# Performance work log

Hardware: AMD Instinct MI355X
Metric: run time of the kernel (lower is better)

The kernel has to match this reference:

```python
import jax, jax.numpy as jnp
import numpy as np

# dims
B, N, D = 256, 77, 768     # batch, CLIP tokens, token dim
K, Dn, H = 16, 768, 8      # nodes, node dim, heads
HID, L = 512, 2            # edge-MLP hidden, num GNN layers


def setup_inputs() -> dict:
    key = jax.random.key(0)
    ks = jax.random.split(key, 12)
    g = lambda k, shape, s=0.02: (jax.random.normal(k, shape, jnp.float32) * s)
    return {
        "w": jax.random.normal(ks[0], (B, N, D), jnp.float32),
        "token_mask": jax.random.randint(ks[1], (B, N), 0, 2).astype(jnp.int32),
        "node_queries": g(ks[2], (1, K, Dn)),
        "Wq": g(ks[3], (Dn, Dn)), "bq": jnp.zeros((Dn,), jnp.float32),
        "Wk": g(ks[4], (D, Dn)),  "bk": jnp.zeros((Dn,), jnp.float32),
        "Wv": g(ks[5], (D, Dn)),  "bv": jnp.zeros((Dn,), jnp.float32),
        "We1": g(ks[6], (2 * Dn, HID)), "be1": jnp.zeros((HID,), jnp.float32),
        "We2": g(ks[7], (HID, 1)),      "be2": jnp.zeros((1,), jnp.float32),
        "fuse_gate": jnp.float32(0.0),
        "Wg": g(ks[8], (L, Dn, Dn)), "bg": jnp.zeros((L, Dn), jnp.float32),
    }


def _edge_logits(V, We1, be1, We2, be2):
    # edge_mlp(cat[Vi, Vj]) without materializing [B,K,K,2Dn]:
    # split first linear into the Vi-half and Vj-half of its weight.
    hi = V @ We1[:Dn]   # [B,K,HID]
    hj = V @ We1[Dn:]   # [B,K,HID]
    h = jax.nn.relu(hi[:, :, None, :] + hj[:, None, :, :] + be1)  # [B,K,K,HID]
    return jnp.einsum('bijh,h->bij', h, We2[:, 0]) + be2[0]       # [B,K,K]


def _forward(w, node_queries, Wq, bq, Wk, bk, Wv, bv,
             We1, be1, We2, be2, fuse_gate, Wg, bg, token_mask):
    q = jnp.broadcast_to(node_queries, (B, K, Dn))
    Q = q @ Wq + bq        # [B,K,Dn]
    Kt = w @ Wk + bk       # [B,N,Dn]
    Vt = w @ Wv + bv       # [B,N,Dn]
    # per-head dot products summed over heads == full Dn dot product
    scale = (Dn // H) ** -0.5
    scores = jnp.einsum('bkd,bnd->bkn', Q, Kt) * scale  # [B,K,N]
    pad = (token_mask == 0)[:, None, :]                 # [B,1,N]
    scores = jnp.where(pad, jnp.finfo(scores.dtype).min, scores)
    # softmax over K per token (transpose to [B,N,K])
    S = jax.nn.softmax(jnp.swapaxes(scores, 1, 2), axis=-1)  # [B,N,K]
    V = jnp.einsum('bnk,bnd->bkd', S, Vt)                    # [B,K,Dn]
    gate = jax.nn.sigmoid(fuse_gate)
    V = (1.0 - gate) * V + gate * q
    # pre-GNN edge logits, then relational GNN refinement
    E = _edge_logits(V, We1, be1, We2, be2)
    A = jax.nn.softmax(E, axis=-1)  # [B,K,K], fixed across layers
    for l in range(L):
        msg = jnp.einsum('bij,bjd->bid', A, V @ Wg[l] + bg[l])
        V = V + jax.nn.relu(msg)
    # post-GNN edge logits
    E = _edge_logits(V, We1, be1, We2, be2)
    return S, V, E


def reference(w, token_mask, node_queries, Wq, bq, Wk, bk, Wv, bv,
              We1, be1, We2, be2, fuse_gate, Wg, bg):
    return _forward(w, node_queries, Wq, bq, Wk, bk, Wv, bv,
                    We1, be1, We2, be2, fuse_gate, Wg, bg, token_mask)
```

## Files before the change

### kernel.cpp

```cpp
#include <hip/hip_runtime.h>

typedef unsigned short u16;
typedef __attribute__((ext_vector_type(8))) short short8;
typedef __attribute__((ext_vector_type(4))) float f32x4;

#define DEV static __device__ __forceinline__

DEV float bf2f(u16 u) { return __uint_as_float(((unsigned)u) << 16); }
DEV u16 f2bf(float f) {
  unsigned u = __float_as_uint(f);
  return (u16)((u + 0x7fffu + ((u >> 16) & 1u)) >> 16);
}

DEV void cp16(void* lds, const void* g) {
  __builtin_amdgcn_global_load_lds(
      (const __attribute__((address_space(1))) unsigned int*)g,
      (__attribute__((address_space(3))) unsigned int*)lds, 16, 0, 0);
}

DEV int xcd_swz() {
  int bid = blockIdx.x;
  int cpx = gridDim.x >> 3;
  return (bid & 7) * cpx + (bid >> 3);
}


__global__ __launch_bounds__(256) void tcast_all(const float* __restrict__ Wv,
                                                 const float* __restrict__ We1,
                                                 const float* __restrict__ Wg,
                                                 u16* __restrict__ WvT,
                                                 u16* __restrict__ We1T,
                                                 u16* __restrict__ WgT) {
  __shared__ float tile[32][33];
  const float* src; u16* dst; int C;
  switch (blockIdx.z) {
    case 0: src = Wv;           dst = WvT;           C = 768; break;
    case 1: src = We1;          dst = We1T;          C = 512; break;
    case 2: src = We1 + 393216; dst = We1T + 393216; C = 512; break;
    case 3: src = Wg;           dst = WgT;           C = 768; break;
    default: src = Wg + 589824; dst = WgT + 589824;  C = 768; break;
  }
  int r0 = blockIdx.y * 32, c0 = blockIdx.x * 32;
  if (c0 >= C) return;
  int tr = threadIdx.x >> 5, tc = threadIdx.x & 31;
#pragma unroll
  for (int rr = 0; rr < 4; ++rr)
    tile[tr + rr * 8][tc] = src[(size_t)(r0 + tr + rr * 8) * C + c0 + tc];
  __syncthreads();
#pragma unroll
  for (int rr = 0; rr < 4; ++rr)
    dst[(size_t)(c0 + tr + rr * 8) * 768 + r0 + tc] = f2bf(tile[tc][tr + rr * 8]);
}

__global__ __launch_bounds__(256) void q_part(const float* __restrict__ nq,
                                              const float* __restrict__ Wq,
                                              float* __restrict__ Qpart) {
  int gid = blockIdx.x * 256 + threadIdx.x;
  int s = blockIdx.y;
  int k = gid / 768, d = gid % 768;
  const float* nr = nq + k * 768 + s * 96;
  const float* wp = Wq + (size_t)(s * 96) * 768 + d;
  float s0 = 0.f, s1 = 0.f, s2 = 0.f, s3 = 0.f;
#pragma unroll
  for (int c = 0; c < 96; c += 4) {
    s0 += nr[c + 0] * wp[(size_t)(c + 0) * 768];
    s1 += nr[c + 1] * wp[(size_t)(c + 1) * 768];
    s2 += nr[c + 2] * wp[(size_t)(c + 2) * 768];
    s3 += nr[c + 3] * wp[(size_t)(c + 3) * 768];
  }
  Qpart[(size_t)s * 12288 + gid] = (s0 + s1) + (s2 + s3);
}

__global__ __launch_bounds__(256) void q_reduce(const float* __restrict__ Qpart,
                                                const float* __restrict__ bq,
                                                float* __restrict__ Qf) {
  int gid = blockIdx.x * 256 + threadIdx.x;
  int d = gid % 768;
  float s = bq[d];
#pragma unroll
  for (int i = 0; i < 8; ++i) s += Qpart[(size_t)i * 12288 + gid];
  Qf[gid] = s;
}

__global__ __launch_bounds__(256) void pt_kernel(const float* __restrict__ Qf,
                                                 const float* __restrict__ Wk,
                                                 const float* __restrict__ bk,
                                                 u16* __restrict__ PT16,
                                                 float* __restrict__ qb) {
  int t = threadIdx.x;
  if (blockIdx.x == 48) {
    int k = t >> 4, j = t & 15;
    const float* q = Qf + k * 768 + j * 48;
    const float* bp = bk + j * 48;
    float s = 0.f;
#pragma unroll
    for (int d = 0; d < 48; d += 4) {
      f32x4 qv = *(const f32x4*)&q[d];
      f32x4 bv4 = *(const f32x4*)&bp[d];
      s += qv[0] * bv4[0] + qv[1] * bv4[1] + qv[2] * bv4[2] + qv[3] * bv4[3];
    }
#pragma unroll
    for (int off = 1; off < 16; off <<= 1) s += __shfl_xor(s, off);
    if (j == 0) qb[k] = s;
    return;
  }
  int gid = blockIdx.x * 256 + t;
  int c = gid >> 4, k = gid & 15;
  const float* wr = Wk + (size_t)c * 768;
  const float* q = Qf + k * 768;
  float s = 0.f;
  for (int d = 0; d < 768; d += 4) {
    f32x4 wv = *(const f32x4*)&wr[d];
    f32x4 qv = *(const f32x4*)&q[d];
    s += wv[0] * qv[0] + wv[1] * qv[1] + wv[2] * qv[2] + wv[3] * qv[3];
  }
  PT16[k * 768 + c] = f2bf(s);
}

__global__ __launch_bounds__(256) void score2(const float* __restrict__ w,
                                              const u16* __restrict__ PT16,
                                              const float* __restrict__ qb,
                                              const int* __restrict__ mask,
                                              float* __restrict__ Sout) {
  __shared__ u16 Ps[16 * 776];
  int t = threadIdx.x, wave = t >> 6, lane = t & 63, l16 = lane & 15, quad = lane >> 4;
  int m0 = blockIdx.x * 64;
#pragma unroll
  for (int r = 0; r < 6; ++r) {
    int idx = t + 256 * r;
    int row = idx / 96, c8 = idx % 96;
    *(short8*)&Ps[row * 776 + c8 * 8] = *(const short8*)&PT16[row * 768 + c8 * 8];
  }
  __syncthreads();
  int row = m0 + wave * 16 + l16;
  const float* ap = w + (size_t)row * 768 + quad * 8;
  f32x4 acc = {0.f, 0.f, 0.f, 0.f};
#pragma unroll
  for (int it = 0; it < 24; ++it) {
    f32x4 a0 = *(const f32x4*)(ap + it * 32);
    f32x4 a1 = *(const f32x4*)(ap + it * 32 + 4);
    short8 fa;
#pragma unroll
    for (int e = 0; e < 4; ++e) { fa[e] = (short)f2bf(a0[e]); fa[e + 4] = (short)f2bf(a1[e]); }
    short8 fb = *(const short8*)&Ps[l16 * 776 + it * 32 + quad * 8];
    acc = __builtin_amdgcn_mfma_f32_16x16x32_bf16(fa, fb, acc, 0, 0, 0);
  }
  float qv = qb[l16];
  const float scale = 0.1020620726159658f;
#pragma unroll
  for (int r = 0; r < 4; ++r) {
    int orow = m0 + wave * 16 + quad * 4 + r;
    float s = (acc[r] + qv) * scale;
    if (mask[orow] == 0) s = -3.402823466e38f;
    float mx = s;
#pragma unroll
    for (int off = 1; off < 16; off <<= 1) mx = fmaxf(mx, __shfl_xor(mx, off));
    float e = __expf(s - mx);
    float sm = e;
#pragma unroll
    for (int off = 1; off < 16; off <<= 1) sm += __shfl_xor(sm, off);
    Sout[(size_t)orow * 16 + l16] = e / sm;
  }
}

__global__ __launch_bounds__(256) void u_kernel(const float* __restrict__ Sg,
                                                const float* __restrict__ w,
                                                u16* __restrict__ U16,
                                                float* __restrict__ sk) {
  __shared__ float Ss[1232];
  int b = blockIdx.x, t = threadIdx.x;
  int d = blockIdx.y * 256 + t;
#pragma unroll
  for (int r = 0; r < 5; ++r) {
    int idx = t + 256 * r;
    if (idx < 1232) Ss[idx] = Sg[(size_t)b * 1232 + idx];
  }
  __syncthreads();
  float a[16];
#pragma unroll
  for (int k = 0; k < 16; ++k) a[k] = 0.f;
  const float* wp = w + (size_t)b * 59136;
  for (int n = 0; n < 77; ++n) {
    float g = wp[(size_t)n * 768 + d];
    const float* sr = &Ss[n * 16];
#pragma unroll
    for (int k = 0; k < 16; ++k) a[k] += sr[k] * g;
  }
#pragma unroll
  for (int k = 0; k < 16; ++k)
    U16[(size_t)b * 12288 + (size_t)k * 768 + d] = f2bf(a[k]);
  if (blockIdx.y == 0 && t < 16) {
    float s = 0.f;
    for (int n = 0; n < 77; ++n) s += Ss[n * 16 + t];
    sk[b * 16 + t] = s;
  }
}

__global__ __launch_bounds__(256) void vgemm(const u16* __restrict__ A,
                                             const u16* __restrict__ BT,
                                             const float* __restrict__ skp,
                                             const float* __restrict__ bv,
                                             const float* __restrict__ nq,
                                             const float* __restrict__ gatep,
                                             float* __restrict__ V32,
                                             u16* __restrict__ V16) {
  __shared__ u16 As[2 * 64 * 32];
  __shared__ u16 Bs[2 * 128 * 32];
  int swz = xcd_swz();
  int mi = swz / 6, ni = swz % 6;
  int m0 = mi * 64, n0 = ni * 128;
  int t = threadIdx.x;
  int wave = t >> 6, lane = t & 63, l16 = lane & 15, quad = lane >> 4;
  int ra = wave * 16 + (lane >> 2);
  int rb1 = wave * 32 + (lane >> 2);
  int rb2 = rb1 + 16;
  int cslot = lane & 3;
  int cga = (cslot ^ ((ra >> 1) & 3)) * 8;
  int cgb1 = (cslot ^ ((rb1 >> 1) & 3)) * 8;
  int cgb2 = (cslot ^ ((rb2 >> 1) & 3)) * 8;

  const u16* Ap = A + (size_t)(m0 + ra) * 768 + cga;
  const u16* Bp1 = BT + (size_t)(n0 + rb1) * 768 + cgb1;
  const u16* Bp2 = BT + (size_t)(n0 + rb2) * 768 + cgb2;
  u16* AsW = &As[(wave * 16) * 32];
  u16* BsW1 = &Bs[(wave * 32) * 32];
  u16* BsW2 = &Bs[(wave * 32 + 16) * 32];

  f32x4 zero4 = {0.f, 0.f, 0.f, 0.f};
  f32x4 acc[4][2];
#pragma unroll
  for (int i = 0; i < 4; ++i) { acc[i][0] = zero4; acc[i][1] = zero4; }

  cp16(AsW, Ap); cp16(BsW1, Bp1); cp16(BsW2, Bp2);

  int cur = 0;
  for (int k0 = 0; k0 < 768; k0 += 32) {
    int nxt = cur ^ 1;
    if (k0 + 32 < 768) {
      cp16(AsW + nxt * 2048, Ap + k0 + 32);
      cp16(BsW1 + nxt * 4096, Bp1 + k0 + 32);
      cp16(BsW2 + nxt * 4096, Bp2 + k0 + 32);
      asm volatile("s_waitcnt vmcnt(3)" ::: "memory");
    } else {
      asm volatile("s_waitcnt vmcnt(0)" ::: "memory");
    }
    asm volatile("s_barrier" ::: "memory");
    const u16* Ab = &As[cur * 2048];
    const u16* Bb = &Bs[cur * 4096];
    short8 fa[4], fb[2];
#pragma unroll
    for (int i = 0; i < 4; ++i) {
      int R = i * 16 + l16;
      fa[i] = *(const short8*)&Ab[R * 32 + (quad ^ ((R >> 1) & 3)) * 8];
    }
#pragma unroll
    for (int j = 0; j < 2; ++j) {
      int R = wave * 32 + j * 16 + l16;
      fb[j] = *(const short8*)&Bb[R * 32 + (quad ^ ((R >> 1) & 3)) * 8];
    }
#pragma unroll
    for (int i = 0; i < 4; ++i)
#pragma unroll
      for (int j = 0; j < 2; ++j)
        acc[i][j] = __builtin_amdgcn_mfma_f32_16x16x32_bf16(fa[i], fb[j], acc[i][j], 0, 0, 0);
    asm volatile("s_barrier" ::: "memory");
    cur = nxt;
  }

  float gv = gatep[0];
  float g = 1.f / (1.f + __expf(-gv)), og = 1.f - g;
  int narr[2]; float bvj[2];
#pragma unroll
  for (int j = 0; j < 2; ++j) {
    narr[j] = n0 + wave * 32 + j * 16 + l16;
    bvj[j] = bv[narr[j]];
  }
#pragma unroll
  for (int i = 0; i < 4; ++i)
#pragma unroll
    for (int r = 0; r < 4; ++r) {
      int m = m0 + i * 16 + quad * 4 + r;
      float skv = skp[m];
      size_t mrow = (size_t)m * 768;
      const float* nqr = nq + (m & 15) * 768;
#pragma unroll
      for (int j = 0; j < 2; ++j) {
        float val = acc[i][j][r] + skv * bvj[j];
        float v = og * val + g * nqr[narr[j]];
        V32[mrow + narr[j]] = v;
        V16[mrow + narr[j]] = f2bf(v);
      }
    }
}

__global__ __launch_bounds__(256) void gemm16s(const u16* __restrict__ A,
                                               const u16* __restrict__ BT0,
                                               const float* __restrict__ bias0,
                                               u16* __restrict__ C0, int N0, int ntA,
                                               const u16* __restrict__ BT1,
                                               const float* __restrict__ bias1,
                                               u16* __restrict__ C1, int N1, int ntB,
                                               int K) {
  __shared__ u16 As[2 * 64 * 32];
  __shared__ u16 Bs[2 * 128 * 32];
  int nt = ntA + ntB;
  int swz = xcd_swz();
  int mi = swz / nt, ni = swz % nt;
  const u16* BT; const float* bias; u16* C; int N, n0;
  if (ni < ntA) { BT = BT0; bias = bias0; C = C0; N = N0; n0 = ni * 128; }
  else          { BT = BT1; bias = bias1; C = C1; N = N1; n0 = (ni - ntA) * 128; }
  int m0 = mi * 64;
  int t = threadIdx.x;
  int wave = t >> 6, lane = t & 63, l16 = lane & 15, quad = lane >> 4;
  int ra = wave * 16 + (lane >> 2);
  int rb1 = wave * 32 + (lane >> 2);
  int rb2 = rb1 + 16;
  int cslot = lane & 3;
  int cga = (cslot ^ ((ra >> 1) & 3)) * 8;
  int cgb1 = (cslot ^ ((rb1 >> 1) & 3)) * 8;
  int cgb2 = (cslot ^ ((rb2 >> 1) & 3)) * 8;

  const u16* Ap = A + (size_t)(m0 + ra) * K + cga;
  const u16* Bp1 = BT + (size_t)(n0 + rb1) * K + cgb1;
  const u16* Bp2 = BT + (size_t)(n0 + rb2) * K + cgb2;
  u16* AsW = &As[(wave * 16) * 32];
  u16* BsW1 = &Bs[(wave * 32) * 32];
  u16* BsW2 = &Bs[(wave * 32 + 16) * 32];

  f32x4 zero4 = {0.f, 0.f, 0.f, 0.f};
  f32x4 acc[4][2];
#pragma unroll
  for (int i = 0; i < 4; ++i) { acc[i][0] = zero4; acc[i][1] = zero4; }

  cp16(AsW, Ap); cp16(BsW1, Bp1); cp16(BsW2, Bp2);

  int cur = 0;
  for (int k0 = 0; k0 < K; k0 += 32) {
    int nxt = cur ^ 1;
    if (k0 + 32 < K) {
      cp16(AsW + nxt * 2048, Ap + k0 + 32);
      cp16(BsW1 + nxt * 4096, Bp1 + k0 + 32);
      cp16(BsW2 + nxt * 4096, Bp2 + k0 + 32);
      asm volatile("s_waitcnt vmcnt(3)" ::: "memory");
    } else {
      asm volatile("s_waitcnt vmcnt(0)" ::: "memory");
    }
    asm volatile("s_barrier" ::: "memory");
    const u16* Ab = &As[cur * 2048];
    const u16* Bb = &Bs[cur * 4096];
    short8 fa[4], fb[2];
#pragma unroll
    for (int i = 0; i < 4; ++i) {
      int R = i * 16 + l16;
      fa[i] = *(const short8*)&Ab[R * 32 + (quad ^ ((R >> 1) & 3)) * 8];
    }
#pragma unroll
    for (int j = 0; j < 2; ++j) {
      int R = wave * 32 + j * 16 + l16;
      fb[j] = *(const short8*)&Bb[R * 32 + (quad ^ ((R >> 1) & 3)) * 8];
    }
#pragma unroll
    for (int i = 0; i < 4; ++i)
#pragma unroll
      for (int j = 0; j < 2; ++j)
        acc[i][j] = __builtin_amdgcn_mfma_f32_16x16x32_bf16(fa[i], fb[j], acc[i][j], 0, 0, 0);
    asm volatile("s_barrier" ::: "memory");
    cur = nxt;
  }

  int narr[2]; float bvj[2];
#pragma unroll
  for (int j = 0; j < 2; ++j) {
    narr[j] = n0 + wave * 32 + j * 16 + l16;
    bvj[j] = bias ? bias[narr[j]] : 0.f;
  }
#pragma unroll
  for (int i = 0; i < 4; ++i)
#pragma unroll
    for (int r = 0; r < 4; ++r) {
      size_t mrow = (size_t)(m0 + i * 16 + quad * 4 + r) * N;
#pragma unroll
      for (int j = 0; j < 2; ++j)
        C[mrow + narr[j]] = f2bf(acc[i][j][r] + bvj[j]);
    }
}

__global__ __launch_bounds__(256) void edge_kernel(const u16* __restrict__ HIJ,
                                                   const float* __restrict__ be1,
                                                   const float* __restrict__ We2,
                                                   const float* __restrict__ be2v,
                                                   float* __restrict__ Aout,
                                                   float* __restrict__ Eout) {
  __shared__ float hiS[8 * 516];
  __shared__ float hjS[16 * 516];
  __shared__ float be1s[512];
  __shared__ float w2s[512];
  int b = blockIdx.x, ih = blockIdx.y, t = threadIdx.x;
  be1s[t] = be1[t]; be1s[t + 256] = be1[t + 256];
  w2s[t] = We2[t];  w2s[t + 256] = We2[t + 256];

#pragma unroll
  for (int r = 0; r < 6; ++r) {
    int idx = t + 256 * r;
    const u16* src;
    float* dst;
    if (idx < 512) {
      int row = idx >> 6, c8 = idx & 63;
      src = &HIJ[(size_t)(b * 16 + ih * 8 + row) * 1024 + c8 * 8];
      dst = &hiS[row * 516 + c8 * 8];
    } else {
      int k = idx - 512;
      int row = k >> 6, c8 = k & 63;
      src = &HIJ[(size_t)(b * 16 + row) * 1024 + 512 + c8 * 8];
      dst = &hjS[row * 516 + c8 * 8];
    }
    short8 hv = *(const short8*)src;
    f32x4 l0, l1;
#pragma unroll
    for (int ee = 0; ee < 4; ++ee) { l0[ee] = bf2f((u16)hv[ee]); l1[ee] = bf2f((u16)hv[ee + 4]); }
    *(f32x4*)dst = l0;
    *(f32x4*)(dst + 4) = l1;
  }
  __syncthreads();

  int i_loc = t >> 5, j = (t >> 1) & 15, hh = t & 1;
  const float* hi = &hiS[i_loc * 516 + hh * 256];
  const float* hj = &hjS[j * 516 + hh * 256];
  const float* b1 = &be1s[hh * 256];
  const float* w2 = &w2s[hh * 256];
  float e = 0.f;
#pragma unroll 2
  for (int h4 = 0; h4 < 64; ++h4) {
    f32x4 hv = *(const f32x4*)&hi[h4 * 4];
    f32x4 jv = *(const f32x4*)&hj[h4 * 4];
    f32x4 bv = *(const f32x4*)&b1[h4 * 4];
    f32x4 wv = *(const f32x4*)&w2[h4 * 4];
#pragma unroll
    for (int ee = 0; ee < 4; ++ee)
      e += fmaxf(hv[ee] + jv[ee] + bv[ee], 0.f) * wv[ee];
  }
  e += __shfl_xor(e, 1);
  e += be2v[0];

  int pair = (ih * 8 + i_loc) * 16 + j;
  if (Aout) {
    float mx = e;
#pragma unroll
    for (int off = 2; off < 32; off <<= 1) mx = fmaxf(mx, __shfl_xor(mx, off));
    float ex = __expf(e - mx);
    float sm = ex;
#pragma unroll
    for (int off = 2; off < 32; off <<= 1) sm += __shfl_xor(sm, off);
    if (hh == 0) Aout[(size_t)b * 256 + pair] = ex / sm;
  }
  if (Eout && hh == 0) Eout[(size_t)b * 256 + pair] = e;
}

__global__ __launch_bounds__(256) void combine_kernel(const float* __restrict__ Aws,
                                                      const u16* __restrict__ G,
                                                      float* __restrict__ V32,
                                                      u16* __restrict__ V16,
                                                      float* __restrict__ Vout) {
  __shared__ float Gs[16 * 260];
  __shared__ float As[256];
  int b = blockIdx.x, yc = blockIdx.y, t = threadIdx.x;
#pragma unroll
  for (int r = 0; r < 2; ++r) {
    int idx = t + 256 * r;
    int row = idx >> 5, c8 = idx & 31;
    short8 gv8 = *(const short8*)&G[(size_t)(b * 16 + row) * 768 + yc * 256 + c8 * 8];
    f32x4 l0, l1;
#pragma unroll
    for (int ee = 0; ee < 4; ++ee) { l0[ee] = bf2f((u16)gv8[ee]); l1[ee] = bf2f((u16)gv8[ee + 4]); }
    *(f32x4*)&Gs[row * 260 + c8 * 8] = l0;
    *(f32x4*)&Gs[row * 260 + c8 * 8 + 4] = l1;
  }
  As[t] = Aws[(size_t)b * 256 + t];
  __syncthreads();
  int d = yc * 256 + t;
  float gv[16];
#pragma unroll
  for (int j = 0; j < 16; ++j) gv[j] = Gs[j * 260 + t];
#pragma unroll
  for (int i = 0; i < 16; ++i) {
    float msg = 0.f;
#pragma unroll
    for (int j = 0; j < 16; ++j) msg += As[i * 16 + j] * gv[j];
    size_t idx = (size_t)b * 12288 + (size_t)i * 768 + d;
    float v = V32[idx] + fmaxf(msg, 0.f);
    V32[idx] = v;
    V16[idx] = f2bf(v);
    if (Vout) Vout[idx] = v;
  }
}

extern "C" void kernel_launch(void* const* d_in, const int* in_sizes, int n_in,
                              void* d_out, int out_size, void* d_ws, size_t ws_size,
                              hipStream_t stream) {
  const float* w    = (const float*)d_in[0];
  const int*   mask = (const int*)d_in[1];
  const float* nq   = (const float*)d_in[2];
  const float* Wq   = (const float*)d_in[3];
  const float* bq   = (const float*)d_in[4];
  const float* Wk   = (const float*)d_in[5];
  const float* bk   = (const float*)d_in[6];
  const float* Wv   = (const float*)d_in[7];
  const float* bv   = (const float*)d_in[8];
  const float* We1  = (const float*)d_in[9];
  const float* be1  = (const float*)d_in[10];
  const float* We2  = (const float*)d_in[11];
  const float* be2  = (const float*)d_in[12];
  const float* gate = (const float*)d_in[13];
  const float* Wg   = (const float*)d_in[14];
  const float* bg   = (const float*)d_in[15];

  float* ws    = (float*)d_ws;
  float* V32   = ws;
  float* Aws   = V32 + 3145728;
  float* Qpart = Aws + 65536;
  float* Qf    = Qpart + 98304;
  float* qb    = Qf + 12288;
  float* sk    = qb + 16;
  u16* PT16    = (u16*)(sk + 4096);
  u16* WvT     = PT16 + 12288;
  u16* We1T    = WvT + 589824;
  u16* WgT     = We1T + 786432;
  u16* V16     = WgT + 1179648;
  u16* U16     = V16 + 3145728;
  u16* HIJ     = U16 + 3145728;
  u16* Gws     = HIJ + 4194304;

  float* out  = (float*)d_out;
  float* Sout = out;
  float* Vout = out + 315392;
  float* Eout = out + 315392 + 3145728;

  dim3 blk(256);

  tcast_all<<<dim3(24, 24, 5), blk, 0, stream>>>(Wv, We1, Wg, WvT, We1T, WgT);
  q_part<<<dim3(48, 8), blk, 0, stream>>>(nq, Wq, Qpart);
  q_reduce<<<48, blk, 0, stream>>>(Qpart, bq, Qf);
  pt_kernel<<<49, blk, 0, stream>>>(Qf, Wk, bk, PT16, qb);

  score2<<<308, blk, 0, stream>>>(w, PT16, qb, mask, Sout);

  u_kernel<<<dim3(256, 3), blk, 0, stream>>>(Sout, w, U16, sk);
  vgemm<<<384, blk, 0, stream>>>(U16, WvT, sk, bv, nq, gate, V32, V16);

  gemm16s<<<896, blk, 0, stream>>>(V16, We1T, nullptr, HIJ, 1024, 8,
                                   WgT, bg, Gws, 768, 6, 768);
  edge_kernel<<<dim3(256, 2), blk, 0, stream>>>(HIJ, be1, We2, be2, Aws, (float*)nullptr);
  combine_kernel<<<dim3(256, 3), blk, 0, stream>>>(Aws, Gws, V32, V16, (float*)nullptr);

  gemm16s<<<384, blk, 0, stream>>>(V16, WgT + 589824, bg + 768, Gws, 768, 6,
                                   WgT + 589824, bg + 768, Gws, 768, 0, 768);
  combine_kernel<<<dim3(256, 3), blk, 0, stream>>>(Aws, Gws, V32, V16, Vout);

  gemm16s<<<512, blk, 0, stream>>>(V16, We1T, nullptr, HIJ, 1024, 8,
                                   We1T, nullptr, HIJ, 1024, 0, 768);
  edge_kernel<<<dim3(256, 2), blk, 0, stream>>>(HIJ, be1, We2, be2, (float*)nullptr, Eout);
}
```

Measured before the change: 307.9 us.

## Enlarge GEMM tiles to 128x128 with deeper prefetch pipeline

The bf16 MFMA GEMMs (V projection, edge-MLP first layer, GNN weight GEMMs) move from 64x128 tiles to 128x128 tiles, with each wave computing a 64x64 sub-block, which doubles A/B reuse per LDS load. The staging also changes: two k-steps are prefetched up front and the next stage is issued after compute, waiting with vmcnt(4). Grid sizes are halved to match. With M=4096, grids shrink to 192-448 blocks, which may underfill the 256 CUs and increases register pressure.

```diff
diff --git a/kernel.cpp b/kernel.cpp
--- a/kernel.cpp
+++ b/kernel.cpp
@@ -196,104 +196,15 @@
   }
 }
 
-__global__ __launch_bounds__(256) void vgemm(const u16* __restrict__ A,
-                                             const u16* __restrict__ BT,
-                                             const float* __restrict__ skp,
-                                             const float* __restrict__ bv,
-                                             const float* __restrict__ nq,
-                                             const float* __restrict__ gatep,
-                                             float* __restrict__ V32,
-                                             u16* __restrict__ V16) {
-  __shared__ u16 As[2 * 64 * 32];
-  __shared__ u16 Bs[2 * 128 * 32];
-  int swz = xcd_swz();
-  int mi = swz / 6, ni = swz % 6;
-  int m0 = mi * 64, n0 = ni * 128;
-  int t = threadIdx.x;
-  int wave = t >> 6, lane = t & 63, l16 = lane & 15, quad = lane >> 4;
-  int ra = wave * 16 + (lane >> 2);
-  int rb1 = wave * 32 + (lane >> 2);
-  int rb2 = rb1 + 16;
-  int cslot = lane & 3;
-  int cga = (cslot ^ ((ra >> 1) & 3)) * 8;
-  int cgb1 = (cslot ^ ((rb1 >> 1) & 3)) * 8;
-  int cgb2 = (cslot ^ ((rb2 >> 1) & 3)) * 8;
-
-  const u16* Ap = A + (size_t)(m0 + ra) * 768 + cga;
-  const u16* Bp1 = BT + (size_t)(n0 + rb1) * 768 + cgb1;
-  const u16* Bp2 = BT + (size_t)(n0 + rb2) * 768 + cgb2;
-  u16* AsW = &As[(wave * 16) * 32];
-  u16* BsW1 = &Bs[(wave * 32) * 32];
-  u16* BsW2 = &Bs[(wave * 32 + 16) * 32];
-
-  f32x4 zero4 = {0.f, 0.f, 0.f, 0.f};
-  f32x4 acc[4][2];
-#pragma unroll
-  for (int i = 0; i < 4; ++i) { acc[i][0] = zero4; acc[i][1] = zero4; }
-
-  cp16(AsW, Ap); cp16(BsW1, Bp1); cp16(BsW2, Bp2);
-
-  int cur = 0;
-  for (int k0 = 0; k0 < 768; k0 += 32) {
-    int nxt = cur ^ 1;
-    if (k0 + 32 < 768) {
-      cp16(AsW + nxt * 2048, Ap + k0 + 32);
-      cp16(BsW1 + nxt * 4096, Bp1 + k0 + 32);
-      cp16(BsW2 + nxt * 4096, Bp2 + k0 + 32);
-      asm volatile("s_waitcnt vmcnt(3)" ::: "memory");
-    } else {
-      asm volatile("s_waitcnt vmcnt(0)" ::: "memory");
-    }
-    asm volatile("s_barrier" ::: "memory");
-    const u16* Ab = &As[cur * 2048];
-    const u16* Bb = &Bs[cur * 4096];
-    short8 fa[4], fb[2];
-#pragma unroll
-    for (int i = 0; i < 4; ++i) {
-      int R = i * 16 + l16;
-      fa[i] = *(const short8*)&Ab[R * 32 + (quad ^ ((R >> 1) & 3)) * 8];
-    }
-#pragma unroll
-    for (int j = 0; j < 2; ++j) {
-      int R = wave * 32 + j * 16 + l16;
-      fb[j] = *(const short8*)&Bb[R * 32 + (quad ^ ((R >> 1) & 3)) * 8];
-    }
-#pragma unroll
-    for (int i = 0; i < 4; ++i)
-#pragma unroll
-      for (int j = 0; j < 2; ++j)
-        acc[i][j] = __builtin_amdgcn_mfma_f32_16x16x32_bf16(fa[i], fb[j], acc[i][j], 0, 0, 0);
-    asm volatile("s_barrier" ::: "memory");
-    cur = nxt;
-  }
-
-  float gv = gatep[0];
-  float g = 1.f / (1.f + __expf(-gv)), og = 1.f - g;
-  int narr[2]; float bvj[2];
-#pragma unroll
-  for (int j = 0; j < 2; ++j) {
-    narr[j] = n0 + wave * 32 + j * 16 + l16;
-    bvj[j] = bv[narr[j]];
-  }
-#pragma unroll
-  for (int i = 0; i < 4; ++i)
-#pragma unroll
-    for (int r = 0; r < 4; ++r) {
-      int m = m0 + i * 16 + quad * 4 + r;
-      float skv = skp[m];
-      size_t mrow = (size_t)m * 768;
-      const float* nqr = nq + (m & 15) * 768;
-#pragma unroll
-      for (int j = 0; j < 2; ++j) {
-        float val = acc[i][j][r] + skv * bvj[j];
-        float v = og * val + g * nqr[narr[j]];
-        V32[mrow + narr[j]] = v;
-        V16[mrow + narr[j]] = f2bf(v);
-      }
-    }
-}
-
-__global__ __launch_bounds__(256) void gemm16s(const u16* __restrict__ A,
+#define STG128(BI, KOFF)                                    \
+  do {                                                      \
+    cp16(&As[(BI) * 4096 + (wave * 32) * 32],      Ap1 + (KOFF)); \
+    cp16(&As[(BI) * 4096 + (wave * 32 + 16) * 32], Ap2 + (KOFF)); \
+    cp16(&Bs[(BI) * 4096 + (wave * 32) * 32],      Bp1 + (KOFF)); \
+    cp16(&Bs[(BI) * 4096 + (wave * 32 + 16) * 32], Bp2 + (KOFF)); \
+  } while (0)
+
+__global__ __launch_bounds__(256) void gemm128(const u16* __restrict__ A,
                                                const u16* __restrict__ BT0,
                                                const float* __restrict__ bias0,
                                                u16* __restrict__ C0, int N0, int ntA,
@@ -301,7 +212,7 @@
                                                const float* __restrict__ bias1,
                                                u16* __restrict__ C1, int N1, int ntB,
                                                int K) {
-  __shared__ u16 As[2 * 64 * 32];
+  __shared__ u16 As[2 * 128 * 32];
   __shared__ u16 Bs[2 * 128 * 32];
   int nt = ntA + ntB;
   int swz = xcd_swz();
@@ -309,79 +220,162 @@
   const u16* BT; const float* bias; u16* C; int N, n0;
   if (ni < ntA) { BT = BT0; bias = bias0; C = C0; N = N0; n0 = ni * 128; }
   else          { BT = BT1; bias = bias1; C = C1; N = N1; n0 = (ni - ntA) * 128; }
-  int m0 = mi * 64;
+  int m0 = mi * 128;
   int t = threadIdx.x;
   int wave = t >> 6, lane = t & 63, l16 = lane & 15, quad = lane >> 4;
-  int ra = wave * 16 + (lane >> 2);
-  int rb1 = wave * 32 + (lane >> 2);
-  int rb2 = rb1 + 16;
+  int wrow = (wave >> 1) * 64, wcol = (wave & 1) * 64;
+  int r1 = wave * 32 + (lane >> 2);
+  int r2 = r1 + 16;
   int cslot = lane & 3;
-  int cga = (cslot ^ ((ra >> 1) & 3)) * 8;
-  int cgb1 = (cslot ^ ((rb1 >> 1) & 3)) * 8;
-  int cgb2 = (cslot ^ ((rb2 >> 1) & 3)) * 8;
-
-  const u16* Ap = A + (size_t)(m0 + ra) * K + cga;
-  const u16* Bp1 = BT + (size_t)(n0 + rb1) * K + cgb1;
-  const u16* Bp2 = BT + (size_t)(n0 + rb2) * K + cgb2;
-  u16* AsW = &As[(wave * 16) * 32];
-  u16* BsW1 = &Bs[(wave * 32) * 32];
-  u16* BsW2 = &Bs[(wave * 32 + 16) * 32];
+  int cg1 = (cslot ^ ((r1 >> 1) & 3)) * 8;
+  int cg2 = (cslot ^ ((r2 >> 1) & 3)) * 8;
+
+  const u16* Ap1 = A + (size_t)(m0 + r1) * K + cg1;
+  const u16* Ap2 = A + (size_t)(m0 + r2) * K + cg2;
+  const u16* Bp1 = BT + (size_t)(n0 + r1) * K + cg1;
+  const u16* Bp2 = BT + (size_t)(n0 + r2) * K + cg2;
 
   f32x4 zero4 = {0.f, 0.f, 0.f, 0.f};
-  f32x4 acc[4][2];
-#pragma unroll
-  for (int i = 0; i < 4; ++i) { acc[i][0] = zero4; acc[i][1] = zero4; }
-
-  cp16(AsW, Ap); cp16(BsW1, Bp1); cp16(BsW2, Bp2);
+  f32x4 acc[4][4];
+#pragma unroll
+  for (int i = 0; i < 4; ++i)
+#pragma unroll
+    for (int j = 0; j < 4; ++j) acc[i][j] = zero4;
+
+  STG128(0, 0); STG128(1, 32);
 
   int cur = 0;
   for (int k0 = 0; k0 < K; k0 += 32) {
-    int nxt = cur ^ 1;
-    if (k0 + 32 < K) {
-      cp16(AsW + nxt * 2048, Ap + k0 + 32);
-      cp16(BsW1 + nxt * 4096, Bp1 + k0 + 32);
-      cp16(BsW2 + nxt * 4096, Bp2 + k0 + 32);
-      asm volatile("s_waitcnt vmcnt(3)" ::: "memory");
-    } else {
-      asm volatile("s_waitcnt vmcnt(0)" ::: "memory");
-    }
+    if (k0 + 32 < K) asm volatile("s_waitcnt vmcnt(4)" ::: "memory");
+    else             asm volatile("s_waitcnt vmcnt(0)" ::: "memory");
     asm volatile("s_barrier" ::: "memory");
-    const u16* Ab = &As[cur * 2048];
+    const u16* Ab = &As[cur * 4096];
     const u16* Bb = &Bs[cur * 4096];
-    short8 fa[4], fb[2];
+    short8 fa[4], fb[4];
 #pragma unroll
     for (int i = 0; i < 4; ++i) {
-      int R = i * 16 + l16;
+      int R = wrow + i * 16 + l16;
       fa[i] = *(const short8*)&Ab[R * 32 + (quad ^ ((R >> 1) & 3)) * 8];
     }
 #pragma unroll
-    for (int j = 0; j < 2; ++j) {
-      int R = wave * 32 + j * 16 + l16;
+    for (int j = 0; j < 4; ++j) {
+      int R = wcol + j * 16 + l16;
       fb[j] = *(const short8*)&Bb[R * 32 + (quad ^ ((R >> 1) & 3)) * 8];
     }
 #pragma unroll
     for (int i = 0; i < 4; ++i)
 #pragma unroll
-      for (int j = 0; j < 2; ++j)
+      for (int j = 0; j < 4; ++j)
         acc[i][j] = __builtin_amdgcn_mfma_f32_16x16x32_bf16(fa[i], fb[j], acc[i][j], 0, 0, 0);
     asm volatile("s_barrier" ::: "memory");
-    cur = nxt;
-  }
-
-  int narr[2]; float bvj[2];
-#pragma unroll
-  for (int j = 0; j < 2; ++j) {
-    narr[j] = n0 + wave * 32 + j * 16 + l16;
+    if (k0 + 64 < K) STG128(cur, k0 + 64);
+    cur ^= 1;
+  }
+
+  int narr[4]; float bvj[4];
+#pragma unroll
+  for (int j = 0; j < 4; ++j) {
+    narr[j] = n0 + wcol + j * 16 + l16;
     bvj[j] = bias ? bias[narr[j]] : 0.f;
   }
 #pragma unroll
   for (int i = 0; i < 4; ++i)
 #pragma unroll
     for (int r = 0; r < 4; ++r) {
-      size_t mrow = (size_t)(m0 + i * 16 + quad * 4 + r) * N;
-#pragma unroll
-      for (int j = 0; j < 2; ++j)
+      size_t mrow = (size_t)(m0 + wrow + i * 16 + quad * 4 + r) * N;
+#pragma unroll
+      for (int j = 0; j < 4; ++j)
         C[mrow + narr[j]] = f2bf(acc[i][j][r] + bvj[j]);
+    }
+}
+
+__global__ __launch_bounds__(256) void vgemm128(const u16* __restrict__ A,
+                                                const u16* __restrict__ BT,
+                                                const float* __restrict__ skp,
+                                                const float* __restrict__ bv,
+                                                const float* __restrict__ nq,
+                                                const float* __restrict__ gatep,
+                                                float* __restrict__ V32,
+                                                u16* __restrict__ V16) {
+  __shared__ u16 As[2 * 128 * 32];
+  __shared__ u16 Bs[2 * 128 * 32];
+  int swz = xcd_swz();
+  int mi = swz / 6, ni = swz % 6;
+  int m0 = mi * 128, n0 = ni * 128;
+  int t = threadIdx.x;
+  int wave = t >> 6, lane = t & 63, l16 = lane & 15, quad = lane >> 4;
+  int wrow = (wave >> 1) * 64, wcol = (wave & 1) * 64;
+  int r1 = wave * 32 + (lane >> 2);
+  int r2 = r1 + 16;
+  int cslot = lane & 3;
+  int cg1 = (cslot ^ ((r1 >> 1) & 3)) * 8;
+  int cg2 = (cslot ^ ((r2 >> 1) & 3)) * 8;
+
+  const u16* Ap1 = A + (size_t)(m0 + r1) * 768 + cg1;
+  const u16* Ap2 = A + (size_t)(m0 + r2) * 768 + cg2;
+  const u16* Bp1 = BT + (size_t)(n0 + r1) * 768 + cg1;
+  const u16* Bp2 = BT + (size_t)(n0 + r2) * 768 + cg2;
+
+  f32x4 zero4 = {0.f, 0.f, 0.f, 0.f};
+  f32x4 acc[4][4];
+#pragma unroll
+  for (int i = 0; i < 4; ++i)
+#pragma unroll
+    for (int j = 0; j < 4; ++j) acc[i][j] = zero4;
+
+  STG128(0, 0); STG128(1, 32);
+
+  int cur = 0;
+  for (int k0 = 0; k0 < 768; k0 += 32) {
+    if (k0 + 32 < 768) asm volatile("s_waitcnt vmcnt(4)" ::: "memory");
+    else               asm volatile("s_waitcnt vmcnt(0)" ::: "memory");
+    asm volatile("s_barrier" ::: "memory");
+    const u16* Ab = &As[cur * 4096];
+    const u16* Bb = &Bs[cur * 4096];
+    short8 fa[4], fb[4];
+#pragma unroll
+    for (int i = 0; i < 4; ++i) {
+      int R = wrow + i * 16 + l16;
+      fa[i] = *(const short8*)&Ab[R * 32 + (quad ^ ((R >> 1) & 3)) * 8];
+    }
+#pragma unroll
+    for (int j = 0; j < 4; ++j) {
+      int R = wcol + j * 16 + l16;
+      fb[j] = *(const short8*)&Bb[R * 32 + (quad ^ ((R >> 1) & 3)) * 8];
+    }
+#pragma unroll
+    for (int i = 0; i < 4; ++i)
+#pragma unroll
+      for (int j = 0; j < 4; ++j)
+        acc[i][j] = __builtin_amdgcn_mfma_f32_16x16x32_bf16(fa[i], fb[j], acc[i][j], 0, 0, 0);
+    asm volatile("s_barrier" ::: "memory");
+    if (k0 + 64 < 768) STG128(cur, k0 + 64);
+    cur ^= 1;
+  }
+
+  float gv = gatep[0];
+  float g = 1.f / (1.f + __expf(-gv)), og = 1.f - g;
+  int narr[4]; float bvj[4];
+#pragma unroll
+  for (int j = 0; j < 4; ++j) {
+    narr[j] = n0 + wcol + j * 16 + l16;
+    bvj[j] = bv[narr[j]];
+  }
+#pragma unroll
+  for (int i = 0; i < 4; ++i)
+#pragma unroll
+    for (int r = 0; r < 4; ++r) {
+      int m = m0 + wrow + i * 16 + quad * 4 + r;
+      float skv = skp[m];
+      size_t mrow = (size_t)m * 768;
+      const float* nqr = nq + (m & 15) * 768;
+#pragma unroll
+      for (int j = 0; j < 4; ++j) {
+        float val = acc[i][j][r] + skv * bvj[j];
+        float v = og * val + g * nqr[narr[j]];
+        V32[mrow + narr[j]] = v;
+        V16[mrow + narr[j]] = f2bf(v);
+      }
     }
 }
 
@@ -545,18 +539,18 @@
   score2<<<308, blk, 0, stream>>>(w, PT16, qb, mask, Sout);
 
   u_kernel<<<dim3(256, 3), blk, 0, stream>>>(Sout, w, U16, sk);
-  vgemm<<<384, blk, 0, stream>>>(U16, WvT, sk, bv, nq, gate, V32, V16);
-
-  gemm16s<<<896, blk, 0, stream>>>(V16, We1T, nullptr, HIJ, 1024, 8,
+  vgemm128<<<192, blk, 0, stream>>>(U16, WvT, sk, bv, nq, gate, V32, V16);
+
+  gemm128<<<448, blk, 0, stream>>>(V16, We1T, nullptr, HIJ, 1024, 8,
                                    WgT, bg, Gws, 768, 6, 768);
   edge_kernel<<<dim3(256, 2), blk, 0, stream>>>(HIJ, be1, We2, be2, Aws, (float*)nullptr);
   combine_kernel<<<dim3(256, 3), blk, 0, stream>>>(Aws, Gws, V32, V16, (float*)nullptr);
 
-  gemm16s<<<384, blk, 0, stream>>>(V16, WgT + 589824, bg + 768, Gws, 768, 6,
+  gemm128<<<192, blk, 0, stream>>>(V16, WgT + 589824, bg + 768, Gws, 768, 6,
                                    WgT + 589824, bg + 768, Gws, 768, 0, 768);
   combine_kernel<<<dim3(256, 3), blk, 0, stream>>>(Aws, Gws, V32, V16, Vout);
 
-  gemm16s<<<512, blk, 0, stream>>>(V16, We1T, nullptr, HIJ, 1024, 8,
+  gemm128<<<256, blk, 0, stream>>>(V16, We1T, nullptr, HIJ, 1024, 8,
                                    We1T, nullptr, HIJ, 1024, 0, 768);
   edge_kernel<<<dim3(256, 2), blk, 0, stream>>>(HIJ, be1, We2, be2, (float*)nullptr, Eout);
 }
```

Measured after the change: 309.3 us. About the same (+0.5%).
